# Kernel tuning notes

Hardware: AMD Instinct MI355X
Metric: run time of the kernel (lower is better)

## Reference

```python
import jax, jax.numpy as jnp
import numpy as np

BN_EPS = 1e-5
SG = jax.lax.stop_gradient


def _silu(z):
    return z * jax.nn.sigmoid(z)


def _binary_activation(x):
    # forward value = sign(x); backward goes through piecewise quadratic out3 (STE)
    out1 = jnp.where(x < -1, -1.0, x * x + 2 * x)
    out2 = jnp.where(x < 0, out1, -x * x + 2 * x)
    out3 = jnp.where(x < 1, out2, 1.0)
    return SG(jnp.sign(x)) - SG(out3) + out3


def _binarize_weight(w):
    # per-output-channel scaling factor * sign(w), STE through clipped weights
    sf = SG(jnp.mean(jnp.abs(w), axis=(1, 2, 3), keepdims=True))  # [O,1,1,1]
    cw = jnp.clip(w, -1.0, 1.0)
    return SG(sf * jnp.sign(w)) - SG(cw) + cw


def _conv3x3_s2(x, w, b):
    y = jax.lax.conv_general_dilated(
        x, w, window_strides=(2, 2), padding=((1, 1), (1, 1)),
        dimension_numbers=("NCHW", "OIHW", "NCHW"))
    return y + b[None, :, None, None]


def _batchnorm_train(x, gamma, beta):
    # training-mode BN: batch statistics over (N,H,W), biased variance
    mean = jnp.mean(x, axis=(0, 2, 3), keepdims=True)
    var = jnp.mean((x - mean) ** 2, axis=(0, 2, 3), keepdims=True)
    xhat = (x - mean) * jax.lax.rsqrt(var + BN_EPS)
    return xhat * gamma[None, :, None, None] + beta[None, :, None, None]


def _learnable_bias(x, emb, w, b):
    # bias = zero_module(linear)(SiLU(emb)) broadcast over H,W
    bias = _silu(emb) @ w.T + b  # [B, C]
    return x + bias[:, :, None, None]


def _avgpool2(x):
    B, C, H, W = x.shape
    return x.reshape(B, C, H // 2, 2, W // 2, 2).mean(axis=(3, 5))


def setup_inputs() -> dict:
    key = jax.random.key(0)
    ks = jax.random.split(key, 16)
    B, Cin, P, E, H, W = 32, 128, 256, 512, 64, 64
    scalor = P // Cin  # 2
    inp = {
        "x": jax.random.normal(ks[0], (B, Cin, H, W), jnp.float32),
        "emb": jax.random.normal(ks[1], (B, E), jnp.float32),
        "m1_w": jax.random.normal(ks[2], (Cin, E), jnp.float32) * 0.02,
        "m1_b": jnp.zeros((Cin,), jnp.float32),
        "conv_w": jax.random.uniform(ks[3], (scalor, Cin, Cin, 3, 3), jnp.float32, -1.0, 1.0) * 0.1,
        "conv_b": jax.random.normal(ks[4], (scalor, Cin), jnp.float32) * 0.01,
        "bn_g": jnp.ones((scalor, Cin), jnp.float32),
        "bn_b": jnp.zeros((scalor, Cin), jnp.float32),
        "m2_w": jax.random.normal(ks[5], (P, E), jnp.float32) * 0.02,
        "m2_b": jnp.zeros((P,), jnp.float32),
        "prelu_a": jnp.full((P,), 0.25, jnp.float32),
        "m3_w": jax.random.normal(ks[6], (P, E), jnp.float32) * 0.02,
        "m3_b": jnp.zeros((P,), jnp.float32),
    }
    return inp


def reference(x, emb, m1_w, m1_b, conv_w, conv_b, bn_g, bn_b,
              m2_w, m2_b, prelu_a, m3_w, m3_b):
    scalor = conv_w.shape[0]
    out = _learnable_bias(x, emb, m1_w, m1_b)
    out = _binary_activation(out)
    xp = _avgpool2(x)  # residual, [B,Cin,H/2,W/2]
    out_list = []
    for i in range(scalor):
        bw = _binarize_weight(conv_w[i])
        y = _conv3x3_s2(out, bw, conv_b[i])
        y = _batchnorm_train(y, bn_g[i], bn_b[i])
        out_list.append(y + xp)
    o = jnp.concatenate(out_list, axis=1)  # [B, planes, H/2, W/2]
    o = _learnable_bias(o, emb, m2_w, m2_b)
    a = prelu_a[None, :, None, None]
    o = jnp.where(o > 0, o, a * o)  # PReLU per channel
    o = _learnable_bias(o, emb, m3_w, m3_b)
    return o
```

## Files before the change

kernel.cpp:

```cpp
#include <hip/hip_runtime.h>
#include <cstdint>
#include <cstddef>

#define B_  32
#define CIN 128
#define P_  256
#define E_  512
#define H_  64
#define W_  64
#define HO  32
#define WO  32

__global__ void k_bw(const float* __restrict__ emb,
                     const float* __restrict__ m1_w, const float* __restrict__ m1_b,
                     const float* __restrict__ m2_w, const float* __restrict__ m2_b,
                     const float* __restrict__ m3_w, const float* __restrict__ m3_b,
                     const float* __restrict__ conv_w,
                     float* __restrict__ b1, float* __restrict__ b2, float* __restrict__ b3,
                     float* __restrict__ sf, unsigned int* __restrict__ wbits,
                     float* __restrict__ s1, float* __restrict__ s2) {
    int bid = blockIdx.x;
    int tid = threadIdx.x;
    int wave = tid >> 6, lane = tid & 63;

    if (bid < B_ * 160) {
        int n = bid / 160, rg = bid % 160;
        int row = rg * 4 + wave;
        const float* sp = emb + n * E_;
        const float* wrow; float bias; float* dst;
        if (row < CIN)            { wrow = m1_w + (size_t)row * E_;          bias = m1_b[row]; dst = b1 + n * CIN + row; }
        else if (row < CIN + P_)  { int c = row - CIN;      wrow = m2_w + (size_t)c * E_; bias = m2_b[c]; dst = b2 + n * P_ + c; }
        else                      { int c = row - CIN - P_; wrow = m3_w + (size_t)c * E_; bias = m3_b[c]; dst = b3 + n * P_ + c; }
        float acc = 0.f;
        #pragma unroll
        for (int j = 0; j < 8; j++) {
            int k = j * 64 + lane;
            float e = sp[k];
            acc += (e / (1.f + expf(-e))) * wrow[k];
        }
        #pragma unroll
        for (int off = 32; off > 0; off >>= 1) acc += __shfl_down(acc, off);
        if (lane == 0) *dst = acc + bias;
        return;
    }

    int base = (bid - B_ * 160) * 2;
    int oc = base + (wave >> 1);
    int iw = wave & 1;
    int i  = iw * 64 + lane;
    if (lane == 0 && iw == 0) { s1[oc] = 0.f; s2[oc] = 0.f; }
    const float* wp = conv_w + ((size_t)oc * CIN + i) * 9;
    float w[9]; float s = 0.f;
    #pragma unroll
    for (int t = 0; t < 9; t++) { w[t] = wp[t]; s += fabsf(w[t]); }
    #pragma unroll
    for (int t = 0; t < 9; t++) {
        unsigned long long m = __ballot(w[t] < 0.f);
        if (lane == 0) {
            wbits[oc * 36 + t * 4 + iw * 2 + 0] = (unsigned int)(m & 0xffffffffull);
            wbits[oc * 36 + t * 4 + iw * 2 + 1] = (unsigned int)(m >> 32);
        }
    }
    #pragma unroll
    for (int off = 32; off > 0; off >>= 1) s += __shfl_down(s, off);
    __shared__ float sred[4];
    if (lane == 0) sred[wave] = s;
    __syncthreads();
    if (tid == 0)        sf[base]     = (sred[0] + sred[1]) / 1152.f;
    else if (tid == 128) sf[base + 1] = (sred[2] + sred[3]) / 1152.f;
}

__global__ void k_prep(const float* __restrict__ x, const float* __restrict__ b1,
                       unsigned int* __restrict__ abits, float* __restrict__ xpool) {
    __shared__ float sb1[CIN];
    int n = blockIdx.x >> 5, h2 = blockIdx.x & 31;
    int tid = threadIdx.x;
    for (int i = tid; i < CIN; i += 256) sb1[i] = b1[n * CIN + i];
    __syncthreads();

    int pix = tid >> 1, half = tid & 1;
    int h = 2 * h2 + (pix >> 6), w = pix & 63;
    const float* xp = x + ((size_t)n * CIN + half * 64) * (H_ * W_) + (size_t)h * W_ + w;
    unsigned int wds[2];
    #pragma unroll
    for (int wd = 0; wd < 2; wd++) {
        unsigned int m = 0;
        #pragma unroll
        for (int b = 0; b < 32; b++) {
            float v = xp[(size_t)(wd * 32 + b) * (H_ * W_)] + sb1[half * 64 + wd * 32 + b];
            m |= (v < 0.f ? 1u : 0u) << b;
        }
        wds[wd] = m;
    }
    ((uint2*)abits)[((size_t)n * 4096 + (size_t)h * 64 + w) * 2 + half] = make_uint2(wds[0], wds[1]);

    for (int idx = tid; idx < CIN * WO; idx += 256) {
        int c = idx >> 5, w2 = idx & 31;
        const float* p = x + ((size_t)n * CIN + c) * (H_ * W_) + (size_t)(2 * h2) * W_ + 2 * w2;
        float2 a = *(const float2*)p;
        float2 b = *(const float2*)(p + W_);
        xpool[((size_t)n * CIN + c) * (HO * WO) + h2 * WO + w2] = 0.25f * (a.x + a.y + b.x + b.y);
    }
}

__global__ void __launch_bounds__(256, 4) k_convstat(const unsigned int* __restrict__ abits,
                                                     const unsigned int* __restrict__ wbits,
                                                     short* __restrict__ y16,
                                                     float* __restrict__ s1, float* __restrict__ s2) {
    __shared__ int red1[32][33], red2[32][33];
    int bid = blockIdx.x;
    int strip = bid & 3, ocg = (bid >> 2) & 7, n = bid >> 5;
    int tid = threadIdx.x;
    int wave = tid >> 6, lane = tid & 63;
    int oh = strip * 8 + (tid >> 5), ow = tid & 31;

    const uint4* asrc = ((const uint4*)abits) + ((size_t)n << 12);
    uint4 img[9]; int vmask = 0;
    #pragma unroll
    for (int kh = 0; kh < 3; kh++) {
        #pragma unroll
        for (int kw = 0; kw < 3; kw++) {
            int t = kh * 3 + kw;
            int r = 2 * oh - 1 + kh, c = 2 * ow - 1 + kw;
            bool v = (unsigned)r < 64u && (unsigned)c < 64u;
            img[t] = v ? asrc[r * 64 + c] : make_uint4(0u, 0u, 0u, 0u);
            vmask |= (v ? 1 : 0) << t;
        }
    }
    int base128 = 128 * __popc(vmask);

    const uint4* wp = ((const uint4*)wbits) + (size_t)ocg * 32 * 9;
    short* yp = y16 + (((size_t)n * P_ + ocg * 32) << 10) + strip * 256 + tid;
    #pragma unroll 4
    for (int o = 0; o < 32; o++) {
        int popsum = 0;
        #pragma unroll
        for (int t = 0; t < 9; t++) {
            uint4 a = img[t];
            uint4 w = wp[o * 9 + t];
            int p = __popc(a.x ^ w.x) + __popc(a.y ^ w.y) +
                    __popc(a.z ^ w.z) + __popc(a.w ^ w.w);
            popsum += ((vmask >> t) & 1) ? p : 0;
        }
        int s = base128 - 2 * popsum;
        yp[(size_t)o << 10] = (short)s;
        int vs = s, v2 = s * s;
        vs += __shfl_down(vs, 32); v2 += __shfl_down(v2, 32);
        vs += __shfl_down(vs, 16); v2 += __shfl_down(v2, 16);
        vs += __shfl_down(vs, 8);  v2 += __shfl_down(v2, 8);
        if (lane < 8) { red1[o][wave * 8 + lane] = vs; red2[o][wave * 8 + lane] = v2; }
    }
    __syncthreads();
    if (tid < 64) {
        int o = tid & 31;
        int a = 0;
        if (tid < 32) {
            #pragma unroll
            for (int p = 0; p < 32; p++) a += red1[o][p];
            atomicAdd(s1 + ocg * 32 + o, (float)a);
        } else {
            #pragma unroll
            for (int p = 0; p < 32; p++) a += red2[o][p];
            atomicAdd(s2 + ocg * 32 + o, (float)a);
        }
    }
}

__global__ void k_epi(const short* __restrict__ y16, const float* __restrict__ xpool,
                      const float* __restrict__ sf,
                      const float* __restrict__ s1, const float* __restrict__ s2,
                      const float* __restrict__ bn_g, const float* __restrict__ bn_b,
                      const float* __restrict__ b2, const float* __restrict__ b3,
                      const float* __restrict__ prelu_a, float* __restrict__ out) {
    int i4 = blockIdx.x * blockDim.x + threadIdx.x;
    int pix4 = i4 & 255;
    int c = (i4 >> 8) & 255;
    int n = i4 >> 16;
    short4 yv = ((const short4*)y16)[i4];
    float4 xv = ((const float4*)xpool)[((n * CIN + (c & 127)) << 8) + pix4];
    const float inv = 1.f / (B_ * HO * WO);
    float sc = sf[c];
    float m = sc * s1[c] * inv;
    float var = fmaf(-m, m, sc * sc * s2[c] * inv);
    float r = rsqrtf(var + 1e-5f) * bn_g[c];
    float add0 = bn_b[c] + b2[n * P_ + c];
    float a = prelu_a[c];
    float b3v = b3[n * P_ + c];
    float o0 = (sc * (float)yv.x - m) * r + add0 + xv.x; o0 = (o0 > 0.f ? o0 : a * o0) + b3v;
    float o1 = (sc * (float)yv.y - m) * r + add0 + xv.y; o1 = (o1 > 0.f ? o1 : a * o1) + b3v;
    float o2 = (sc * (float)yv.z - m) * r + add0 + xv.z; o2 = (o2 > 0.f ? o2 : a * o2) + b3v;
    float o3 = (sc * (float)yv.w - m) * r + add0 + xv.w; o3 = (o3 > 0.f ? o3 : a * o3) + b3v;
    ((float4*)out)[i4] = make_float4(o0, o1, o2, o3);
}

extern "C" void kernel_launch(void* const* d_in, const int* in_sizes, int n_in,
                              void* d_out, int out_size, void* d_ws, size_t ws_size,
                              hipStream_t stream) {
    const float* x      = (const float*)d_in[0];
    const float* emb    = (const float*)d_in[1];
    const float* m1_w   = (const float*)d_in[2];
    const float* m1_b   = (const float*)d_in[3];
    const float* conv_w = (const float*)d_in[4];
    const float* bn_g   = (const float*)d_in[6];
    const float* bn_b   = (const float*)d_in[7];
    const float* m2_w   = (const float*)d_in[8];
    const float* m2_b   = (const float*)d_in[9];
    const float* prelu_a= (const float*)d_in[10];
    const float* m3_w   = (const float*)d_in[11];
    const float* m3_b   = (const float*)d_in[12];

    float* out = (float*)d_out;

    float* wsf = (float*)d_ws;
    float* b1    = wsf;
    float* b2    = wsf + 4096;
    float* b3    = wsf + 12288;
    float* sf    = wsf + 20480;
    float* s1    = wsf + 20736;
    float* s2    = wsf + 20992;
    unsigned int* wbits = (unsigned int*)(wsf + 21248);
    unsigned int* abits = (unsigned int*)(wsf + 30464);
    float* xpool = wsf + 554752;
    short* y16   = (short*)(wsf + 4749056 + 16384);

    k_bw      <<<B_ * 160 + P_ / 2, 256, 0, stream>>>(emb, m1_w, m1_b, m2_w, m2_b, m3_w, m3_b,
                                                      conv_w, b1, b2, b3, sf, wbits, s1, s2);
    k_prep    <<<B_ * 32, 256, 0, stream>>>(x, b1, abits, xpool);
    k_convstat<<<B_ * 32, 256, 0, stream>>>(abits, wbits, y16, s1, s2);
    k_epi     <<<(B_ * P_ * HO * WO) / (4 * 256), 256, 0, stream>>>(y16, xpool, sf, s1, s2,
                                                                    bn_g, bn_b, b2, b3, prelu_a, out);
}
```

Before: 190.4 us.

## Pad binary activation grid and correct borders with precomputed weight sums

Activation bitplanes are now stored in a zero-padded 65x65 grid, so the conv kernel loads all nine taps without bounds checks. A small per-channel table is computed in the weight kernel: the top-row, left-column and corner tap sums of the signed weights. The conv kernel uses it to subtract the contribution that padded zero taps would otherwise add, in place of per-tap validity masking. This removes branches and selects from the inner popcount loop. In exchange the prep kernel writes padding borders and the weight kernel does extra work.

```diff
diff --git a/kernel.cpp b/kernel.cpp
--- a/kernel.cpp
+++ b/kernel.cpp
@@ -10,6 +10,8 @@
 #define W_  64
 #define HO  32
 #define WO  32
+#define PS  65
+#define PN  4225
 
 __global__ void k_bw(const float* __restrict__ emb,
                      const float* __restrict__ m1_w, const float* __restrict__ m1_b,
@@ -18,7 +20,10 @@
                      const float* __restrict__ conv_w,
                      float* __restrict__ b1, float* __restrict__ b2, float* __restrict__ b3,
                      float* __restrict__ sf, unsigned int* __restrict__ wbits,
+                     int4* __restrict__ ctab,
                      float* __restrict__ s1, float* __restrict__ s2) {
+    __shared__ float sred[4];
+    __shared__ int spop[4][9];
     int bid = blockIdx.x;
     int tid = threadIdx.x;
     int wave = tid >> 6, lane = tid & 63;
@@ -59,15 +64,26 @@
         if (lane == 0) {
             wbits[oc * 36 + t * 4 + iw * 2 + 0] = (unsigned int)(m & 0xffffffffull);
             wbits[oc * 36 + t * 4 + iw * 2 + 1] = (unsigned int)(m >> 32);
+            spop[wave][t] = __popcll(m);
         }
     }
     #pragma unroll
     for (int off = 32; off > 0; off >>= 1) s += __shfl_down(s, off);
-    __shared__ float sred[4];
     if (lane == 0) sred[wave] = s;
     __syncthreads();
-    if (tid == 0)        sf[base]     = (sred[0] + sred[1]) / 1152.f;
-    else if (tid == 128) sf[base + 1] = (sred[2] + sred[3]) / 1152.f;
+    if (tid == 0) {
+        sf[base]     = (sred[0] + sred[1]) / 1152.f;
+        sf[base + 1] = (sred[2] + sred[3]) / 1152.f;
+        #pragma unroll
+        for (int j = 0; j < 2; j++) {
+            int tv[9];
+            #pragma unroll
+            for (int t = 0; t < 9; t++) tv[t] = 128 - 2 * (spop[2 * j][t] + spop[2 * j + 1][t]);
+            int Cr = tv[0] + tv[1] + tv[2];
+            int Cc = tv[0] + tv[3] + tv[6];
+            ctab[base + j] = make_int4(Cr, Cc, tv[0], 0);
+        }
+    }
 }
 
 __global__ void k_prep(const float* __restrict__ x, const float* __restrict__ b1,
@@ -76,6 +92,10 @@
     int n = blockIdx.x >> 5, h2 = blockIdx.x & 31;
     int tid = threadIdx.x;
     for (int i = tid; i < CIN; i += 256) sb1[i] = b1[n * CIN + i];
+
+    uint4* ab4 = ((uint4*)abits) + (size_t)n * PN;
+    if (h2 == 0 && tid < PS) ab4[tid] = make_uint4(0u, 0u, 0u, 0u);
+    if (tid < 2) ab4[(2 * h2 + 1 + tid) * PS] = make_uint4(0u, 0u, 0u, 0u);
     __syncthreads();
 
     int pix = tid >> 1, half = tid & 1;
@@ -92,7 +112,7 @@
         }
         wds[wd] = m;
     }
-    ((uint2*)abits)[((size_t)n * 4096 + (size_t)h * 64 + w) * 2 + half] = make_uint2(wds[0], wds[1]);
+    ((uint2*)abits)[((size_t)n * PN + (size_t)(h + 1) * PS + (w + 1)) * 2 + half] = make_uint2(wds[0], wds[1]);
 
     for (int idx = tid; idx < CIN * WO; idx += 256) {
         int c = idx >> 5, w2 = idx & 31;
@@ -105,6 +125,7 @@
 
 __global__ void __launch_bounds__(256, 4) k_convstat(const unsigned int* __restrict__ abits,
                                                      const unsigned int* __restrict__ wbits,
+                                                     const int4* __restrict__ ctab,
                                                      short* __restrict__ y16,
                                                      float* __restrict__ s1, float* __restrict__ s2) {
     __shared__ int red1[32][33], red2[32][33];
@@ -114,22 +135,20 @@
     int wave = tid >> 6, lane = tid & 63;
     int oh = strip * 8 + (tid >> 5), ow = tid & 31;
 
-    const uint4* asrc = ((const uint4*)abits) + ((size_t)n << 12);
-    uint4 img[9]; int vmask = 0;
-    #pragma unroll
-    for (int kh = 0; kh < 3; kh++) {
-        #pragma unroll
-        for (int kw = 0; kw < 3; kw++) {
-            int t = kh * 3 + kw;
-            int r = 2 * oh - 1 + kh, c = 2 * ow - 1 + kw;
-            bool v = (unsigned)r < 64u && (unsigned)c < 64u;
-            img[t] = v ? asrc[r * 64 + c] : make_uint4(0u, 0u, 0u, 0u);
-            vmask |= (v ? 1 : 0) << t;
-        }
-    }
-    int base128 = 128 * __popc(vmask);
+    const uint4* ab = ((const uint4*)abits) + (size_t)n * PN + (size_t)(2 * oh) * PS + 2 * ow;
+    uint4 img[9];
+    #pragma unroll
+    for (int kh = 0; kh < 3; kh++)
+        #pragma unroll
+        for (int kw = 0; kw < 3; kw++)
+            img[kh * 3 + kw] = ab[kh * PS + kw];
+
+    int fr = (oh == 0) ? -1 : 0;
+    int fc = (ow == 0) ? -1 : 0;
+    int f0 = fr & fc;
 
     const uint4* wp = ((const uint4*)wbits) + (size_t)ocg * 32 * 9;
+    const int4* cp = ctab + ocg * 32;
     short* yp = y16 + (((size_t)n * P_ + ocg * 32) << 10) + strip * 256 + tid;
     #pragma unroll 4
     for (int o = 0; o < 32; o++) {
@@ -138,11 +157,11 @@
         for (int t = 0; t < 9; t++) {
             uint4 a = img[t];
             uint4 w = wp[o * 9 + t];
-            int p = __popc(a.x ^ w.x) + __popc(a.y ^ w.y) +
-                    __popc(a.z ^ w.z) + __popc(a.w ^ w.w);
-            popsum += ((vmask >> t) & 1) ? p : 0;
-        }
-        int s = base128 - 2 * popsum;
+            popsum += __popc(a.x ^ w.x) + __popc(a.y ^ w.y) +
+                      __popc(a.z ^ w.z) + __popc(a.w ^ w.w);
+        }
+        int4 C = cp[o];
+        int s = 1152 - 2 * popsum - (fr & C.x) - (fc & C.y) + (f0 & C.z);
         yp[(size_t)o << 10] = (short)s;
         int vs = s, v2 = s * s;
         vs += __shfl_down(vs, 32); v2 += __shfl_down(v2, 32);
@@ -218,15 +237,16 @@
     float* sf    = wsf + 20480;
     float* s1    = wsf + 20736;
     float* s2    = wsf + 20992;
-    unsigned int* wbits = (unsigned int*)(wsf + 21248);
-    unsigned int* abits = (unsigned int*)(wsf + 30464);
-    float* xpool = wsf + 554752;
-    short* y16   = (short*)(wsf + 4749056 + 16384);
+    int4*  ctab  = (int4*)(wsf + 21248);
+    unsigned int* wbits = (unsigned int*)(wsf + 22272);
+    unsigned int* abits = (unsigned int*)(wsf + 31488);
+    float* xpool = wsf + 572288;
+    short* y16   = (short*)(wsf + 4766592);
 
     k_bw      <<<B_ * 160 + P_ / 2, 256, 0, stream>>>(emb, m1_w, m1_b, m2_w, m2_b, m3_w, m3_b,
-                                                      conv_w, b1, b2, b3, sf, wbits, s1, s2);
+                                                      conv_w, b1, b2, b3, sf, wbits, ctab, s1, s2);
     k_prep    <<<B_ * 32, 256, 0, stream>>>(x, b1, abits, xpool);
-    k_convstat<<<B_ * 32, 256, 0, stream>>>(abits, wbits, y16, s1, s2);
+    k_convstat<<<B_ * 32, 256, 0, stream>>>(abits, wbits, ctab, y16, s1, s2);
     k_epi     <<<(B_ * P_ * HO * WO) / (4 * 256), 256, 0, stream>>>(y16, xpool, sf, s1, s2,
                                                                     bn_g, bn_b, b2, b3, prelu_a, out);
 }
```

Measured after the change: 190.8 us. No clear change (+0.2%).
